# Kernel optimization log

Hardware: AMD Instinct MI355X
Metric: run time of the kernel (lower is better)

Reference implementation:

```python
import jax, jax.numpy as jnp
import numpy as np

B, T, S, E, H, D = 4, 1024, 1024, 1024, 16, 64


def _ln(x, g, b, eps=1e-5):
    m = x.mean(-1, keepdims=True)
    v = ((x - m) ** 2).mean(-1, keepdims=True)
    return (x - m) * jax.lax.rsqrt(v + eps) * g + b


def _mha(xq, xkv, mask4, Wq, Wk, Wv, Wo, bo):
    # Wq/Wk/Wv: [H, E, D] (stacked per-head bias-free linears)
    q = jnp.einsum('bte,hed->bhtd', xq, Wq)
    k = jnp.einsum('bse,hed->bhsd', xkv, Wk)
    v = jnp.einsum('bse,hed->bhsd', xkv, Wv)
    # NOTE: original scales by C**-0.5 with C = n_embd, not head_size
    wei = jnp.einsum('bhtd,bhsd->bhts', q, k) * (float(E) ** -0.5)
    wei = jnp.where(mask4 == 0, jnp.float32(-1e9), wei)
    wei = jax.nn.softmax(wei, axis=-1)
    o = jnp.einsum('bhts,bhsd->bhtd', wei, v)  # [B,H,T,D]
    b_, h_, t_, d_ = o.shape
    o = o.transpose(0, 2, 1, 3).reshape(b_, t_, h_ * d_)
    return o @ Wo + bo


def setup_inputs() -> dict:
    key = jax.random.key(0)
    ks = jax.random.split(key, 24)
    sd = 0.02
    inp = {
        'x': jax.random.normal(ks[0], (B, T, E), jnp.float32),
        'x_m': jnp.ones((B, 1, T), jnp.int32),
        'ca': jax.random.normal(ks[1], (B, S, E), jnp.float32),
        'ca_m': jnp.ones((B, 1, S), jnp.int32),
        'Wq_s': jax.random.normal(ks[2], (H, E, D), jnp.float32) * sd,
        'Wk_s': jax.random.normal(ks[3], (H, E, D), jnp.float32) * sd,
        'Wv_s': jax.random.normal(ks[4], (H, E, D), jnp.float32) * sd,
        'Wo_s': jax.random.normal(ks[5], (E, E), jnp.float32) * sd,
        'bo_s': jnp.zeros((E,), jnp.float32),
        'Wq_c': jax.random.normal(ks[6], (H, E, D), jnp.float32) * sd,
        'Wk_c': jax.random.normal(ks[7], (H, E, D), jnp.float32) * sd,
        'Wv_c': jax.random.normal(ks[8], (H, E, D), jnp.float32) * sd,
        'Wo_c': jax.random.normal(ks[9], (E, E), jnp.float32) * sd,
        'bo_c': jnp.zeros((E,), jnp.float32),
        'ln1_g': jnp.ones((E,), jnp.float32), 'ln1_b': jnp.zeros((E,), jnp.float32),
        'ln2_g': jnp.ones((E,), jnp.float32), 'ln2_b': jnp.zeros((E,), jnp.float32),
        'ln3_g': jnp.ones((E,), jnp.float32), 'ln3_b': jnp.zeros((E,), jnp.float32),
        'W1': jax.random.normal(ks[10], (E, 4 * E), jnp.float32) * sd,
        'b1': jnp.zeros((4 * E,), jnp.float32),
        'W2': jax.random.normal(ks[11], (4 * E, E), jnp.float32) * sd,
        'b2': jnp.zeros((E,), jnp.float32),
    }
    return inp


def reference(x, x_m, ca, ca_m, Wq_s, Wk_s, Wv_s, Wo_s, bo_s,
              Wq_c, Wk_c, Wv_c, Wo_c, bo_c,
              ln1_g, ln1_b, ln2_g, ln2_b, ln3_g, ln3_b,
              W1, b1, W2, b2):
    tril = jnp.tril(jnp.ones((T, T), jnp.int32))
    # self-attn mask: x_m [B,1,T] & tril [T,T] -> [B,1,T,T] (broadcast over heads)
    self_mask = x_m[:, :, None, :] * tril          # [B,1,T,T]
    cross_mask = ca_m[:, :, None, :]               # [B,1,1,S]
    x = x + _mha(_ln(x, ln1_g, ln1_b), _ln(x, ln1_g, ln1_b) if False else _ln(x, ln1_g, ln1_b), self_mask, Wq_s, Wk_s, Wv_s, Wo_s, bo_s)
    x = x + _mha(_ln(x, ln2_g, ln2_b), ca, cross_mask, Wq_c, Wk_c, Wv_c, Wo_c, bo_c)
    h = _ln(x, ln3_g, ln3_b)
    x = x + (jax.nn.relu(h @ W1 + b1) @ W2 + b2)
    return x
```

## Files before the change

### kernel.cpp

```cpp
#include <hip/hip_runtime.h>
#include <hip/hip_bf16.h>
#include <cstdint>
#include <cstddef>

typedef __attribute__((ext_vector_type(8))) short  s8v;
typedef __attribute__((ext_vector_type(4))) short  s4v;
typedef __attribute__((ext_vector_type(8))) __bf16 b8v;
typedef __attribute__((ext_vector_type(4))) float  f32x4;
typedef __attribute__((ext_vector_type(4))) unsigned u32x4;

__device__ __forceinline__ short f2bf(float f){
  unsigned u = __builtin_bit_cast(unsigned, f);
  unsigned r = (u + 0x7fffu + ((u >> 16) & 1u)) >> 16;
  return (short)(unsigned short)r;
}
__device__ __forceinline__ float bf2f(short s){
  return __builtin_bit_cast(float, ((unsigned)(unsigned short)s) << 16);
}

__device__ __forceinline__ f32x4 mfma16(s8v a, s8v b, f32x4 c){
  return __builtin_amdgcn_mfma_f32_16x16x32_bf16(
      __builtin_bit_cast(b8v, a), __builtin_bit_cast(b8v, b), c, 0, 0, 0);
}

__device__ __forceinline__ unsigned cvtpk(float a, float b){
  unsigned w;
  asm("v_cvt_pk_bf16_f32 %0, %1, %2" : "=v"(w) : "v"(a), "v"(b));
  return w;
}

__global__ __launch_bounds__(256)
void ln_k(const float* __restrict__ x, const float* __restrict__ g,
          const float* __restrict__ b, short* __restrict__ out)
{
  const int row = blockIdx.x, tid = threadIdx.x;
  const float4 v = ((const float4*)(x + (size_t)row*1024))[tid];
  float s  = v.x+v.y+v.z+v.w;
  float s2 = v.x*v.x+v.y*v.y+v.z*v.z+v.w*v.w;
  #pragma unroll
  for (int off=32; off; off>>=1){ s += __shfl_down(s, off); s2 += __shfl_down(s2, off); }
  __shared__ float red[8];
  const int wave = tid>>6, lane = tid&63;
  if (lane==0){ red[wave]=s; red[4+wave]=s2; }
  __syncthreads();
  s  = red[0]+red[1]+red[2]+red[3];
  s2 = red[4]+red[5]+red[6]+red[7];
  const float mean = s*(1.f/1024.f);
  const float rstd = rsqrtf(s2*(1.f/1024.f) - mean*mean + 1e-5f);
  const float4 gv = ((const float4*)g)[tid];
  const float4 bv = ((const float4*)b)[tid];
  s4v o;
  o[0] = f2bf((v.x-mean)*rstd*gv.x + bv.x);
  o[1] = f2bf((v.y-mean)*rstd*gv.y + bv.y);
  o[2] = f2bf((v.z-mean)*rstd*gv.z + bv.z);
  o[3] = f2bf((v.w-mean)*rstd*gv.w + bv.w);
  *(s4v*)(out + (size_t)row*1024 + tid*4) = o;
}

__global__ __launch_bounds__(256)
void cast_k(const float* __restrict__ in, short* __restrict__ out)
{
  const int i = blockIdx.x*256 + threadIdx.x;
  const float4 v = ((const float4*)in)[i];
  s4v o; o[0]=f2bf(v.x); o[1]=f2bf(v.y); o[2]=f2bf(v.z); o[3]=f2bf(v.w);
  ((s4v*)out)[i] = o;
}

__global__ __launch_bounds__(256)
void tcast_k(const float* __restrict__ in, short* __restrict__ out, int E2, int D2)
{
  __shared__ float t[32][33];
  const int h  = blockIdx.z;
  const int e0 = blockIdx.x*32, d0 = blockIdx.y*32;
  const int tx = threadIdx.x & 31, ty = threadIdx.x >> 5;
  const float* ip = in + (size_t)h*E2*D2;
  #pragma unroll
  for (int r = ty; r < 32; r += 8)
    t[r][tx] = ip[(size_t)(e0+r)*D2 + d0 + tx];
  __syncthreads();
  short* op = out + (size_t)h*D2*E2;
  #pragma unroll
  for (int r = ty; r < 32; r += 8)
    op[(size_t)(d0+r)*E2 + e0 + tx] = f2bf(t[tx][r]);
}

__global__ __launch_bounds__(256)
void vtrans_k(const short* __restrict__ V, int ldv, short* __restrict__ Vt, int S, int H)
{
  __shared__ short t[32][34];
  const int bh = blockIdx.z;
  const int b = bh / H, h = bh % H;
  const int s0 = blockIdx.x*32, d0 = blockIdx.y*32;
  const int tx = threadIdx.x & 31, ty = threadIdx.x >> 5;
  const short* ip = V + (size_t)b*S*ldv + h*64;
  #pragma unroll
  for (int r = ty; r < 32; r += 8)
    t[r][tx] = ip[(size_t)(s0+r)*ldv + d0 + tx];
  __syncthreads();
  short* op = Vt + ((size_t)bh*64 + d0)*S + s0;
  #pragma unroll
  for (int r = ty; r < 32; r += 8)
    op[(size_t)r*S + tx] = t[tx][r];
}

__global__ __launch_bounds__(256)
void red4_k(const short* __restrict__ p, const float* __restrict__ bias,
            const float* __restrict__ resid, float* __restrict__ out)
{
  const int i = blockIdx.x*256 + threadIdx.x;
  float4 o = ((const float4*)resid)[i];
  const float4 bv = ((const float4*)bias)[i & 255];
  o.x += bv.x; o.y += bv.y; o.z += bv.z; o.w += bv.w;
  #pragma unroll
  for (int z=0; z<4; z++){
    const s4v v = ((const s4v*)(p + (size_t)z*4194304))[i];
    o.x += bf2f(v[0]); o.y += bf2f(v[1]); o.z += bf2f(v[2]); o.w += bf2f(v[3]);
  }
  ((float4*)out)[i] = o;
}

template<int BN, int BIAS, int RELU, int RESID, int WF32>
__global__ __launch_bounds__(256, 2)
void gemm_bt(const short* __restrict__ A, const short* __restrict__ Bt,
             const float* __restrict__ bias, const float* __restrict__ resid,
             short* __restrict__ Cb, float* __restrict__ Cf,
             int M, int N, int K)
{
  __shared__ short lds[3][128*32 + BN*32];
  const int nwg = gridDim.x * gridDim.y;
  int id = blockIdx.y * gridDim.x + blockIdx.x;
  id = (id & 7) * (nwg >> 3) + (id >> 3);
  const int bx = id % gridDim.x, by = id / gridDim.x;
  const int m0 = by*128, n0 = bx*BN;

  const int tid  = threadIdx.x;
  const int wave = tid>>6, lane = tid&63;
  const int lo = lane&15, hi = lane>>4;
  const int wm = wave>>1, wn = wave&1;

  constexpr int NJ = BN/32;
  constexpr int BC = BN>>6;
  f32x4 acc[4][NJ] = {};
  const int NK = K >> 5;

  auto stage = [&](int buf, int kt){
    const short* Ag = A  + (size_t)m0*K + kt*32;
    const short* Bg = Bt + (size_t)n0*K + kt*32;
    #pragma unroll
    for (int c=0;c<2;c++){
      const int q = (wave*2+c)*64 + lane;
      const int r = q>>2, cc = q&3;
      __builtin_amdgcn_global_load_lds(
        (const __attribute__((address_space(1))) void*)(Ag + (size_t)r*K + cc*8),
        (__attribute__((address_space(3))) void*)(&lds[buf][(wave*2+c)*512]),
        16, 0, 0);
    }
    #pragma unroll
    for (int c=0;c<BC;c++){
      const int q = (wave*BC+c)*64 + lane;
      const int r = q>>2, cc = q&3;
      __builtin_amdgcn_global_load_lds(
        (const __attribute__((address_space(1))) void*)(Bg + (size_t)r*K + cc*8),
        (__attribute__((address_space(3))) void*)(&lds[buf][4096 + (wave*BC+c)*512]),
        16, 0, 0);
    }
  };

  stage(0, 0);
  if (NK > 1) stage(1, 1);

  for (int kt=0; kt<NK; kt++){
    if (kt+1 < NK){
      if constexpr (BN==128) asm volatile("s_waitcnt vmcnt(4)" ::: "memory");
      else                   asm volatile("s_waitcnt vmcnt(3)" ::: "memory");
    } else {
      asm volatile("s_waitcnt vmcnt(0)" ::: "memory");
    }
    __builtin_amdgcn_s_barrier();
    __builtin_amdgcn_sched_barrier(0);
    if (kt+2 < NK) stage((kt+2)%3, kt+2);

    const short* la = &lds[kt%3][0];
    const short* lb = &lds[kt%3][4096];
    s8v af[4], bfr[NJ];
    #pragma unroll
    for (int i=0;i<4;i++)
      af[i] = *(const s8v*)(la + (wm*64 + i*16 + lo)*32 + hi*8);
    #pragma unroll
    for (int j=0;j<NJ;j++)
      bfr[j] = *(const s8v*)(lb + (wn*(BN/2) + j*16 + lo)*32 + hi*8);
    #pragma unroll
    for (int i=0;i<4;i++)
      #pragma unroll
      for (int j=0;j<NJ;j++)
        acc[i][j] = mfma16(af[i], bfr[j], acc[i][j]);
  }

  #pragma unroll
  for (int i=0;i<4;i++){
    const int row = m0 + wm*64 + i*16 + hi*4;
    #pragma unroll
    for (int j=0;j<NJ;j++){
      const int col = n0 + wn*(BN/2) + j*16 + lo;
      const float bv = BIAS ? bias[col] : 0.0f;
      #pragma unroll
      for (int r=0;r<4;r++){
        float v = acc[i][j][r] + bv;
        if (RELU) v = fmaxf(v, 0.0f);
        const size_t idx = (size_t)(row + r)*N + col;
        if (RESID) v += resid[idx];
        if (WF32) Cf[idx] = v; else Cb[idx] = f2bf(v);
      }
    }
  }
}

template<int BIAS, int RELU, int RESID, int WF32>
__global__ __launch_bounds__(512, 1)
void gemm256(const short* __restrict__ A, int lda,
             const short* __restrict__ Bt, int ldb,
             const float* __restrict__ bias, const float* __restrict__ resid,
             short* __restrict__ Cb, float* __restrict__ Cf,
             int M, int N, int K)
{
  __shared__ short lds[2][32768];
  const int nwg = gridDim.x * gridDim.y;
  int id = blockIdx.y * gridDim.x + blockIdx.x;
  id = (id & 7) * (nwg >> 3) + (id >> 3);
  const int bx = id % gridDim.x, by = id / gridDim.x;
  const int m0 = by*256, n0 = bx*256;
  A  += (size_t)blockIdx.z * K;
  Bt += (size_t)blockIdx.z * K;
  const size_t cofs = (size_t)blockIdx.z * M * N;

  const int tid = threadIdx.x;
  const int lane = tid&63, wave = tid>>6;
  const int lo = lane&15, hi = lane>>4;
  const int wr = wave>>2, wc = wave&3;

  f32x4 acc[8][4] = {};
  const int NT = K >> 6;

  auto stageA = [&](int buf, int kt, int part){
    const short* Ag = A + (size_t)m0*lda + kt*64;
    const int q = part*512 + tid;
    const int r = q>>3, c = q&7;
    __builtin_amdgcn_global_load_lds(
      (const __attribute__((address_space(1))) void*)(Ag + (size_t)r*lda + ((c^(r&7))*8)),
      (__attribute__((address_space(3))) void*)(&lds[buf][q*8]), 16, 0, 0);
  };
  auto stageB = [&](int buf, int kt, int part){
    const short* Bg = Bt + (size_t)n0*ldb + kt*64;
    const int q = part*512 + tid;
    const int r = q>>3, c = q&7;
    __builtin_amdgcn_global_load_lds(
      (const __attribute__((address_space(1))) void*)(Bg + (size_t)r*ldb + ((c^(r&7))*8)),
      (__attribute__((address_space(3))) void*)(&lds[buf][16384 + q*8]), 16, 0, 0);
  };

  #pragma unroll
  for (int p=0;p<4;p++){ stageA(0,0,p); stageB(0,0,p); }
  __syncthreads();

  for (int t=0; t<NT; t++){
    const int cur = t&1;
    const short* la = &lds[cur][0];
    const short* lb = &lds[cur][16384];
    const bool pf = (t+1 < NT);
    #pragma unroll
    for (int ks=0; ks<2; ks++){
      s8v bf[4];
      #pragma unroll
      for (int j=0;j<4;j++){
        const int r = wc*64 + j*16 + lo;
        bf[j] = *(const s8v*)(lb + r*64 + (((ks*4+hi)^(r&7))*8));
      }
      #pragma unroll
      for (int mh=0; mh<2; mh++){
        s8v af[4];
        #pragma unroll
        for (int i=0;i<4;i++){
          const int r = wr*128 + mh*64 + i*16 + lo;
          af[i] = *(const s8v*)(la + r*64 + (((ks*4+hi)^(r&7))*8));
        }
        if (pf && ks==0){
          stageA(cur^1, t+1, mh*2);   stageB(cur^1, t+1, mh*2);
          stageA(cur^1, t+1, mh*2+1); stageB(cur^1, t+1, mh*2+1);
        }
        __builtin_amdgcn_s_setprio(1);
        #pragma unroll
        for (int i=0;i<4;i++)
          #pragma unroll
          for (int j=0;j<4;j++)
            acc[mh*4+i][j] = mfma16(af[i], bf[j], acc[mh*4+i][j]);
        __builtin_amdgcn_s_setprio(0);
      }
    }
    __syncthreads();
  }

  #pragma unroll
  for (int I=0;I<8;I++){
    const int row = m0 + wr*128 + I*16 + hi*4;
    #pragma unroll
    for (int j=0;j<4;j++){
      const int col = n0 + wc*64 + j*16 + lo;
      const float bv = BIAS ? bias[col] : 0.0f;
      #pragma unroll
      for (int r=0;r<4;r++){
        float v = acc[I][j][r] + bv;
        if (RELU) v = fmaxf(v, 0.0f);
        const size_t idx = cofs + (size_t)(row + r)*N + col;
        if (RESID) v += resid[idx];
        if (WF32) Cf[idx] = v; else Cb[idx] = f2bf(v);
      }
    }
  }
}

template<int CAUSAL>
__global__ __launch_bounds__(256, 4)
void attn_k(const short* __restrict__ Q, int ldq,
            const short* __restrict__ K, int ldk,
            const short* __restrict__ Vt, int ldvt,
            const int* __restrict__ msk,
            short* __restrict__ O, int ldo,
            int H, int Tq, int Sk)
{
  __shared__ short kls[2][4096];
  __shared__ short vls[2][4096];
  const int bh = blockIdx.x;
  const int b = bh / H, h = bh % H;
  const int tid = threadIdx.x;
  const int wave = tid>>6, lane = tid&63;
  const int lo = lane&15, hi = lane>>4;
  const int t0 = blockIdx.y*64 + wave*16;

  const short* Qb  = Q + (size_t)(b*Tq)*ldq + h*64;
  const short* Kb  = K + (size_t)(b*Sk)*ldk + h*64;
  const short* Vtb = Vt + (size_t)bh*64*ldvt;
  const int*   mb  = msk + (size_t)b*Sk;

  const short* qp = Qb + (size_t)(t0+lo)*ldq + hi*8;
  const s8v qa0 = *(const s8v*)(qp);
  const s8v qa1 = *(const s8v*)(qp + 32);

  float mrow = -INFINITY, lrow = 0.f;
  f32x4 oacc[4] = {};
  const int trow = t0 + lo;
  const int nblk = CAUSAL ? (blockIdx.y + 1) : (Sk>>6);
  const float sc2 = 0.03125f * 1.44269504088896f;
  const int x8 = lo & 7;

  auto stage = [&](int buf, int it){
    const int s0 = it*64;
    #pragma unroll
    for (int rd=0; rd<2; rd++){
      const int q = rd*256 + tid;
      const int r = q>>3, c = q&7;
      const int cs = (c ^ (r&7))*8;
      __builtin_amdgcn_global_load_lds(
        (const __attribute__((address_space(1))) void*)(Kb + (size_t)(s0+r)*ldk + cs),
        (__attribute__((address_space(3))) void*)(&kls[buf][(rd*256 + wave*64)*8]),
        16, 0, 0);
      __builtin_amdgcn_global_load_lds(
        (const __attribute__((address_space(1))) void*)(Vtb + (size_t)r*ldvt + s0 + cs),
        (__attribute__((address_space(3))) void*)(&vls[buf][(rd*256 + wave*64)*8]),
        16, 0, 0);
    }
  };

  stage(0, 0);
  int cur = 0;
  for (int it=0; it<nblk; it++){
    __syncthreads();
    if (it+1 < nblk) stage(cur^1, it+1);
    const int s0 = it*64;

    int ka[4][4];
    #pragma unroll
    for (int g=0; g<4; g++){
      const int4 kv = ((const int4*)mb)[(s0>>2) + g*4 + hi];
      ka[g][0]=kv.x; ka[g][1]=kv.y; ka[g][2]=kv.z; ka[g][3]=kv.w;
    }

    const short* kl = kls[cur];
    s8v kf[4][2];
    #pragma unroll
    for (int g=0; g<4; g++){
      const int rb = (g*16 + lo)*64;
      kf[g][0] = *(const s8v*)(kl + rb + ((hi     ^ x8)*8));
      kf[g][1] = *(const s8v*)(kl + rb + (((4+hi) ^ x8)*8));
    }

    f32x4 sg[4] = {};
    __builtin_amdgcn_s_setprio(1);
    #pragma unroll
    for (int g=0; g<4; g++){
      sg[g] = mfma16(kf[g][0], qa0, sg[g]);
      sg[g] = mfma16(kf[g][1], qa1, sg[g]);
    }
    __builtin_amdgcn_s_setprio(0);

    const bool lastblk = CAUSAL && (it == nblk-1);
    float p[4][4];
    #pragma unroll
    for (int g=0; g<4; g++)
      #pragma unroll
      for (int r=0; r<4; r++){
        const int sidx = s0 + g*16 + 4*hi + r;
        const bool ok = ka[g][r] && (!lastblk || sidx <= trow);
        p[g][r] = ok ? sg[g][r]*sc2 : -1.5e9f;
      }

    float bmax;
    {
      float m0_ = fmaxf(fmaxf(p[0][0],p[0][1]), fmaxf(p[0][2],p[0][3]));
      float m1_ = fmaxf(fmaxf(p[1][0],p[1][1]), fmaxf(p[1][2],p[1][3]));
      float m2_ = fmaxf(fmaxf(p[2][0],p[2][1]), fmaxf(p[2][2],p[2][3]));
      float m3_ = fmaxf(fmaxf(p[3][0],p[3][1]), fmaxf(p[3][2],p[3][3]));
      bmax = fmaxf(fmaxf(m0_,m1_), fmaxf(m2_,m3_));
    }
    bmax = fmaxf(bmax, __shfl_xor(bmax, 16));
    bmax = fmaxf(bmax, __shfl_xor(bmax, 32));

    const float mn  = fmaxf(mrow, bmax);
    const float fac = exp2f(mrow - mn);
    mrow = mn;
    #pragma unroll
    for (int g=0; g<4; g++)
      #pragma unroll
      for (int r=0; r<4; r++)
        p[g][r] = exp2f(p[g][r] - mn);

    float bsum;
    {
      float s0_ = (p[0][0]+p[0][1]) + (p[0][2]+p[0][3]);
      float s1_ = (p[1][0]+p[1][1]) + (p[1][2]+p[1][3]);
      float s2_ = (p[2][0]+p[2][1]) + (p[2][2]+p[2][3]);
      float s3_ = (p[3][0]+p[3][1]) + (p[3][2]+p[3][3]);
      bsum = (s0_+s1_) + (s2_+s3_);
    }
    bsum += __shfl_xor(bsum, 16);
    bsum += __shfl_xor(bsum, 32);
    lrow = lrow*fac + bsum;
    #pragma unroll
    for (int f=0; f<4; f++)
      #pragma unroll
      for (int r=0; r<4; r++)
        oacc[f][r] *= fac;

    u32x4 pw0, pw1;
    pw0[0] = cvtpk(p[0][0], p[0][1]);
    pw0[1] = cvtpk(p[0][2], p[0][3]);
    pw0[2] = cvtpk(p[1][0], p[1][1]);
    pw0[3] = cvtpk(p[1][2], p[1][3]);
    pw1[0] = cvtpk(p[2][0], p[2][1]);
    pw1[1] = cvtpk(p[2][2], p[2][3]);
    pw1[2] = cvtpk(p[3][0], p[3][1]);
    pw1[3] = cvtpk(p[3][2], p[3][3]);
    const s8v pb0 = __builtin_bit_cast(s8v, pw0);
    const s8v pb1 = __builtin_bit_cast(s8v, pw1);

    const short* vl = vls[cur];
    __builtin_amdgcn_s_setprio(1);
    #pragma unroll
    for (int f=0; f<4; f++){
      const int rb = (f*16 + lo)*64;
      const int h2 = hi>>1, o2 = (hi&1)*4;
      const s4v a0 = *(const s4v*)(vl + rb + (((h2  ) ^ x8)*8) + o2);
      const s4v a1 = *(const s4v*)(vl + rb + (((2+h2) ^ x8)*8) + o2);
      const s4v a2 = *(const s4v*)(vl + rb + (((4+h2) ^ x8)*8) + o2);
      const s4v a3 = *(const s4v*)(vl + rb + (((6+h2) ^ x8)*8) + o2);
      const s8v av0 = __builtin_shufflevector(a0, a1, 0,1,2,3,4,5,6,7);
      const s8v av1 = __builtin_shufflevector(a2, a3, 0,1,2,3,4,5,6,7);
      oacc[f] = mfma16(av0, pb0, oacc[f]);
      oacc[f] = mfma16(av1, pb1, oacc[f]);
    }
    __builtin_amdgcn_s_setprio(0);
    cur ^= 1;
  }

  const float inv = 1.0f / lrow;
  short* Ob = O + (size_t)(b*Tq)*ldo + h*64 + (size_t)(t0+lo)*ldo + 4*hi;
  #pragma unroll
  for (int f=0; f<4; f++){
    s4v o;
    #pragma unroll
    for (int r=0; r<4; r++) o[r] = f2bf(oacc[f][r]*inv);
    *(s4v*)(Ob + f*16) = o;
  }
}

extern "C" void kernel_launch(void* const* d_in, const int* in_sizes, int n_in,
                              void* d_out, int out_size, void* d_ws, size_t ws_size,
                              hipStream_t stream)
{
  (void)in_sizes; (void)n_in; (void)out_size; (void)ws_size;
  const float* x    = (const float*)d_in[0];
  const int*   xm   = (const int*)  d_in[1];
  const float* ca   = (const float*)d_in[2];
  const int*   cam  = (const int*)  d_in[3];
  const float* Wq_s = (const float*)d_in[4];
  const float* Wk_s = (const float*)d_in[5];
  const float* Wv_s = (const float*)d_in[6];
  const float* Wo_s = (const float*)d_in[7];
  const float* bo_s = (const float*)d_in[8];
  const float* Wq_c = (const float*)d_in[9];
  const float* Wk_c = (const float*)d_in[10];
  const float* Wv_c = (const float*)d_in[11];
  const float* Wo_c = (const float*)d_in[12];
  const float* bo_c = (const float*)d_in[13];
  const float* ln1g = (const float*)d_in[14];
  const float* ln1b = (const float*)d_in[15];
  const float* ln2g = (const float*)d_in[16];
  const float* ln2b = (const float*)d_in[17];
  const float* ln3g = (const float*)d_in[18];
  const float* ln3b = (const float*)d_in[19];
  const float* W1   = (const float*)d_in[20];
  const float* b1   = (const float*)d_in[21];
  const float* W2   = (const float*)d_in[22];
  const float* b2   = (const float*)d_in[23];
  float* out = (float*)d_out;

  char* ws = (char*)d_ws;
  size_t off = 0;
  auto alloc = [&](size_t bytes)->void*{
    void* p = ws + off; off += (bytes + 255) & ~(size_t)255; return p; };

  short* w_qkv_s = (short*)alloc((size_t)3072*1024*2);
  short* w_o_s   = (short*)alloc((size_t)1024*1024*2);
  short* w_q_c   = (short*)alloc((size_t)1024*1024*2);
  short* w_kv_c  = (short*)alloc((size_t)2048*1024*2);
  short* w_o_c   = (short*)alloc((size_t)1024*1024*2);
  short* w_1     = (short*)alloc((size_t)4096*1024*2);
  short* w_2     = (short*)alloc((size_t)1024*4096*2);
  short* xn      = (short*)alloc((size_t)4096*1024*2);
  short* cab     = (short*)alloc((size_t)4096*1024*2);
  short* qkv     = (short*)alloc((size_t)4096*3072*2);
  short* attno   = (short*)alloc((size_t)4096*1024*2);
  float* xres    = (float*)alloc((size_t)4096*1024*4);
  short* hffn    = (short*)alloc((size_t)4096*4096*2);
  float* pA      = (float*)alloc((size_t)4096*1024*4);
  float* pB      = (float*)alloc((size_t)4096*1024*4);
  short* pP      = (short*)pA;
  short* kvbuf   = qkv + (size_t)4096*1024;
  short* vt_s    = hffn;
  short* vt_c    = hffn + (size_t)4*1024*1024;
  (void)pB;

  tcast_k<<<dim3(32,  2,16),256,0,stream>>>(Wq_s, w_qkv_s,           1024,   64);
  tcast_k<<<dim3(32,  2,16),256,0,stream>>>(Wk_s, w_qkv_s+1024*1024, 1024,   64);
  tcast_k<<<dim3(32,  2,16),256,0,stream>>>(Wv_s, w_qkv_s+2048*1024, 1024,   64);
  tcast_k<<<dim3(32, 32, 1),256,0,stream>>>(Wo_s, w_o_s,             1024, 1024);
  tcast_k<<<dim3(32,  2,16),256,0,stream>>>(Wq_c, w_q_c,             1024,   64);
  tcast_k<<<dim3(32,  2,16),256,0,stream>>>(Wk_c, w_kv_c,            1024,   64);
  tcast_k<<<dim3(32,  2,16),256,0,stream>>>(Wv_c, w_kv_c+1024*1024,  1024,   64);
  tcast_k<<<dim3(32, 32, 1),256,0,stream>>>(Wo_c, w_o_c,             1024, 1024);
  tcast_k<<<dim3(32,128, 1),256,0,stream>>>(W1,   w_1,               1024, 4096);
  tcast_k<<<dim3(128,32, 1),256,0,stream>>>(W2,   w_2,               4096, 1024);
  cast_k<<<4096,256,0,stream>>>(ca, cab);

  ln_k<<<4096,256,0,stream>>>(x, ln1g, ln1b, xn);
  gemm256<0,0,0,0><<<dim3(12,16),512,0,stream>>>(xn, 1024, w_qkv_s, 1024,
                                                 nullptr, nullptr, qkv, nullptr,
                                                 4096, 3072, 1024);
  vtrans_k<<<dim3(32,2,64),256,0,stream>>>(qkv+2048, 3072, vt_s, 1024, 16);
  attn_k<1><<<dim3(64,16),256,0,stream>>>(qkv, 3072, qkv+1024, 3072, vt_s, 1024,
                                          xm, attno, 1024, 16, 1024, 1024);
  gemm_bt<64,1,0,1,1><<<dim3(16,32),256,0,stream>>>(attno, w_o_s, bo_s, x,
                                                    nullptr, xres, 4096, 1024, 1024);

  ln_k<<<4096,256,0,stream>>>(xres, ln2g, ln2b, xn);
  gemm_bt<64,0,0,0,0><<<dim3(16,32),256,0,stream>>>(xn, w_q_c, nullptr, nullptr,
                                                    qkv, nullptr, 4096, 1024, 1024);
  gemm256<0,0,0,0><<<dim3(8,16),512,0,stream>>>(cab, 1024, w_kv_c, 1024,
                                                nullptr, nullptr, kvbuf, nullptr,
                                                4096, 2048, 1024);
  vtrans_k<<<dim3(32,2,64),256,0,stream>>>(kvbuf+1024, 2048, vt_c, 1024, 16);
  attn_k<0><<<dim3(64,16),256,0,stream>>>(qkv, 1024, kvbuf, 2048, vt_c, 1024,
                                          cam, attno, 1024, 16, 1024, 1024);
  gemm_bt<64,1,0,1,1><<<dim3(16,32),256,0,stream>>>(attno, w_o_c, bo_c, xres,
                                                    nullptr, xres, 4096, 1024, 1024);

  ln_k<<<4096,256,0,stream>>>(xres, ln3g, ln3b, xn);
  gemm256<1,1,0,0><<<dim3(16,16),512,0,stream>>>(xn, 1024, w_1, 1024,
                                                 b1, nullptr, hffn, nullptr,
                                                 4096, 4096, 1024);
  gemm256<0,0,0,0><<<dim3(4,16,4),512,0,stream>>>(hffn, 4096, w_2, 4096,
                                                  nullptr, nullptr, pP, nullptr,
                                                  4096, 1024, 1024);
  red4_k<<<4096,256,0,stream>>>(pP, b2, xres, out);
}
```

Baseline: 378.9 us.

## Fold softmax scale into Q GEMMs, precompute mask bias, lazy rescale, permute Vt

Folds the attention scale times log2(e) into the Q projection epilogues, so the attention loop no longer multiplies scores by the scale. The integer key mask is converted once into an additive float bias, and the causal check now runs only on the last block. Online-softmax rescaling of the accumulators is skipped unless the block max exceeds the running max by more than 8, which lets p values grow up to 2^8 before renormalisation. V transpose writes a permuted column order so the PV MFMA operands load as single 8-wide vectors instead of four 4-wide loads plus shuffles. These remove per-element ALU and LDS work from the attention inner loop, in exchange for a tighter reliance on fp32 headroom and a Q buffer stored pre-scaled in bf16.

```diff
diff --git a/kernel.cpp b/kernel.cpp
--- a/kernel.cpp
+++ b/kernel.cpp
@@ -8,6 +8,8 @@
 typedef __attribute__((ext_vector_type(8))) __bf16 b8v;
 typedef __attribute__((ext_vector_type(4))) float  f32x4;
 typedef __attribute__((ext_vector_type(4))) unsigned u32x4;
+
+#define SC2Q 0.0450843293f
 
 __device__ __forceinline__ short f2bf(float f){
   unsigned u = __builtin_bit_cast(unsigned, f);
@@ -67,6 +69,15 @@
 }
 
 __global__ __launch_bounds__(256)
+void mkb_k(const int* __restrict__ xm, const int* __restrict__ cm,
+           float* __restrict__ mbS, float* __restrict__ mbC)
+{
+  const int i = blockIdx.x*256 + threadIdx.x;
+  mbS[i] = xm[i] ? 0.f : -1.5e9f;
+  mbC[i] = cm[i] ? 0.f : -1.5e9f;
+}
+
+__global__ __launch_bounds__(256)
 void tcast_k(const float* __restrict__ in, short* __restrict__ out, int E2, int D2)
 {
   __shared__ float t[32][33];
@@ -97,10 +108,13 @@
   for (int r = ty; r < 32; r += 8)
     t[r][tx] = ip[(size_t)(s0+r)*ldv + d0 + tx];
   __syncthreads();
-  short* op = Vt + ((size_t)bh*64 + d0)*S + s0;
+  const int s  = s0 + tx;
+  const int ks = (s>>5)&1, bb = (tx>>4)&1, hh = (tx>>2)&3, rr = tx&3;
+  const int cp = (s & ~63) + ks*32 + hh*8 + bb*4 + rr;
+  short* op = Vt + ((size_t)bh*64 + d0)*S;
   #pragma unroll
   for (int r = ty; r < 32; r += 8)
-    op[(size_t)r*S + tx] = t[tx][r];
+    op[(size_t)r*S + cp] = t[tx][r];
 }
 
 __global__ __launch_bounds__(256)
@@ -119,7 +133,7 @@
   ((float4*)out)[i] = o;
 }
 
-template<int BN, int BIAS, int RELU, int RESID, int WF32>
+template<int BN, int BIAS, int RELU, int RESID, int WF32, int SCQ>
 __global__ __launch_bounds__(256, 2)
 void gemm_bt(const short* __restrict__ A, const short* __restrict__ Bt,
              const float* __restrict__ bias, const float* __restrict__ resid,
@@ -206,6 +220,7 @@
       #pragma unroll
       for (int r=0;r<4;r++){
         float v = acc[i][j][r] + bv;
+        if constexpr (SCQ==2) v *= SC2Q;
         if (RELU) v = fmaxf(v, 0.0f);
         const size_t idx = (size_t)(row + r)*N + col;
         if (RESID) v += resid[idx];
@@ -215,7 +230,7 @@
   }
 }
 
-template<int BIAS, int RELU, int RESID, int WF32>
+template<int BIAS, int RELU, int RESID, int WF32, int SCQ>
 __global__ __launch_bounds__(512, 1)
 void gemm256(const short* __restrict__ A, int lda,
              const short* __restrict__ Bt, int ldb,
@@ -309,6 +324,7 @@
       #pragma unroll
       for (int r=0;r<4;r++){
         float v = acc[I][j][r] + bv;
+        if constexpr (SCQ==1) { if (col < 1024) v *= SC2Q; }
         if (RELU) v = fmaxf(v, 0.0f);
         const size_t idx = cofs + (size_t)(row + r)*N + col;
         if (RESID) v += resid[idx];
@@ -323,7 +339,7 @@
 void attn_k(const short* __restrict__ Q, int ldq,
             const short* __restrict__ K, int ldk,
             const short* __restrict__ Vt, int ldvt,
-            const int* __restrict__ msk,
+            const float* __restrict__ mbias,
             short* __restrict__ O, int ldo,
             int H, int Tq, int Sk)
 {
@@ -339,7 +355,7 @@
   const short* Qb  = Q + (size_t)(b*Tq)*ldq + h*64;
   const short* Kb  = K + (size_t)(b*Sk)*ldk + h*64;
   const short* Vtb = Vt + (size_t)bh*64*ldvt;
-  const int*   mb  = msk + (size_t)b*Sk;
+  const float* mb  = mbias + (size_t)b*Sk;
 
   const short* qp = Qb + (size_t)(t0+lo)*ldq + hi*8;
   const s8v qa0 = *(const s8v*)(qp);
@@ -349,7 +365,6 @@
   f32x4 oacc[4] = {};
   const int trow = t0 + lo;
   const int nblk = CAUSAL ? (blockIdx.y + 1) : (Sk>>6);
-  const float sc2 = 0.03125f * 1.44269504088896f;
   const int x8 = lo & 7;
 
   auto stage = [&](int buf, int it){
@@ -377,13 +392,6 @@
     if (it+1 < nblk) stage(cur^1, it+1);
     const int s0 = it*64;
 
-    int ka[4][4];
-    #pragma unroll
-    for (int g=0; g<4; g++){
-      const int4 kv = ((const int4*)mb)[(s0>>2) + g*4 + hi];
-      ka[g][0]=kv.x; ka[g][1]=kv.y; ka[g][2]=kv.z; ka[g][3]=kv.w;
-    }
-
     const short* kl = kls[cur];
     s8v kf[4][2];
     #pragma unroll
@@ -402,53 +410,63 @@
     }
     __builtin_amdgcn_s_setprio(0);
 
-    const bool lastblk = CAUSAL && (it == nblk-1);
     float p[4][4];
     #pragma unroll
-    for (int g=0; g<4; g++)
-      #pragma unroll
-      for (int r=0; r<4; r++){
-        const int sidx = s0 + g*16 + 4*hi + r;
-        const bool ok = ka[g][r] && (!lastblk || sidx <= trow);
-        p[g][r] = ok ? sg[g][r]*sc2 : -1.5e9f;
-      }
+    for (int g=0; g<4; g++){
+      const f32x4 mv = ((const f32x4*)mb)[(s0>>2) + g*4 + hi];
+      #pragma unroll
+      for (int r=0; r<4; r++)
+        p[g][r] = sg[g][r] + mv[r];
+    }
+    if (CAUSAL && it == nblk-1){
+      #pragma unroll
+      for (int g=0; g<4; g++)
+        #pragma unroll
+        for (int r=0; r<4; r++){
+          const int sidx = s0 + g*16 + 4*hi + r;
+          if (sidx > trow) p[g][r] = -1.5e9f;
+        }
+    }
 
     float bmax;
     {
-      float m0_ = fmaxf(fmaxf(p[0][0],p[0][1]), fmaxf(p[0][2],p[0][3]));
-      float m1_ = fmaxf(fmaxf(p[1][0],p[1][1]), fmaxf(p[1][2],p[1][3]));
-      float m2_ = fmaxf(fmaxf(p[2][0],p[2][1]), fmaxf(p[2][2],p[2][3]));
-      float m3_ = fmaxf(fmaxf(p[3][0],p[3][1]), fmaxf(p[3][2],p[3][3]));
+      const float m0_ = fmaxf(fmaxf(fmaxf(p[0][0],p[0][1]),p[0][2]),p[0][3]);
+      const float m1_ = fmaxf(fmaxf(fmaxf(p[1][0],p[1][1]),p[1][2]),p[1][3]);
+      const float m2_ = fmaxf(fmaxf(fmaxf(p[2][0],p[2][1]),p[2][2]),p[2][3]);
+      const float m3_ = fmaxf(fmaxf(fmaxf(p[3][0],p[3][1]),p[3][2]),p[3][3]);
       bmax = fmaxf(fmaxf(m0_,m1_), fmaxf(m2_,m3_));
     }
     bmax = fmaxf(bmax, __shfl_xor(bmax, 16));
     bmax = fmaxf(bmax, __shfl_xor(bmax, 32));
 
-    const float mn  = fmaxf(mrow, bmax);
-    const float fac = exp2f(mrow - mn);
-    mrow = mn;
-    #pragma unroll
-    for (int g=0; g<4; g++)
-      #pragma unroll
-      for (int r=0; r<4; r++)
-        p[g][r] = exp2f(p[g][r] - mn);
+    if (!__all(bmax <= mrow + 8.0f)){
+      const float mn  = fmaxf(mrow, bmax);
+      const float fac = exp2f(mrow - mn);
+      mrow = mn;
+      lrow *= fac;
+      #pragma unroll
+      for (int f=0; f<4; f++)
+        #pragma unroll
+        for (int r=0; r<4; r++)
+          oacc[f][r] *= fac;
+    }
 
     float bsum;
     {
-      float s0_ = (p[0][0]+p[0][1]) + (p[0][2]+p[0][3]);
-      float s1_ = (p[1][0]+p[1][1]) + (p[1][2]+p[1][3]);
-      float s2_ = (p[2][0]+p[2][1]) + (p[2][2]+p[2][3]);
-      float s3_ = (p[3][0]+p[3][1]) + (p[3][2]+p[3][3]);
+      #pragma unroll
+      for (int g=0; g<4; g++)
+        #pragma unroll
+        for (int r=0; r<4; r++)
+          p[g][r] = exp2f(p[g][r] - mrow);
+      const float s0_ = (p[0][0]+p[0][1]) + (p[0][2]+p[0][3]);
+      const float s1_ = (p[1][0]+p[1][1]) + (p[1][2]+p[1][3]);
+      const float s2_ = (p[2][0]+p[2][1]) + (p[2][2]+p[2][3]);
+      const float s3_ = (p[3][0]+p[3][1]) + (p[3][2]+p[3][3]);
       bsum = (s0_+s1_) + (s2_+s3_);
     }
     bsum += __shfl_xor(bsum, 16);
     bsum += __shfl_xor(bsum, 32);
-    lrow = lrow*fac + bsum;
-    #pragma unroll
-    for (int f=0; f<4; f++)
-      #pragma unroll
-      for (int r=0; r<4; r++)
-        oacc[f][r] *= fac;
+    lrow += bsum;
 
     u32x4 pw0, pw1;
     pw0[0] = cvtpk(p[0][0], p[0][1]);
@@ -467,13 +485,8 @@
     #pragma unroll
     for (int f=0; f<4; f++){
       const int rb = (f*16 + lo)*64;
-      const int h2 = hi>>1, o2 = (hi&1)*4;
-      const s4v a0 = *(const s4v*)(vl + rb + (((h2  ) ^ x8)*8) + o2);
-      const s4v a1 = *(const s4v*)(vl + rb + (((2+h2) ^ x8)*8) + o2);
-      const s4v a2 = *(const s4v*)(vl + rb + (((4+h2) ^ x8)*8) + o2);
-      const s4v a3 = *(const s4v*)(vl + rb + (((6+h2) ^ x8)*8) + o2);
-      const s8v av0 = __builtin_shufflevector(a0, a1, 0,1,2,3,4,5,6,7);
-      const s8v av1 = __builtin_shufflevector(a2, a3, 0,1,2,3,4,5,6,7);
+      const s8v av0 = *(const s8v*)(vl + rb + (((hi  ) ^ x8)*8));
+      const s8v av1 = *(const s8v*)(vl + rb + (((4+hi) ^ x8)*8));
       oacc[f] = mfma16(av0, pb0, oacc[f]);
       oacc[f] = mfma16(av1, pb1, oacc[f]);
     }
@@ -543,6 +556,8 @@
   short* hffn    = (short*)alloc((size_t)4096*4096*2);
   float* pA      = (float*)alloc((size_t)4096*1024*4);
   float* pB      = (float*)alloc((size_t)4096*1024*4);
+  float* mbS     = (float*)alloc((size_t)4096*4);
+  float* mbC     = (float*)alloc((size_t)4096*4);
   short* pP      = (short*)pA;
   short* kvbuf   = qkv + (size_t)4096*1024;
   short* vt_s    = hffn;
@@ -560,35 +575,36 @@
   tcast_k<<<dim3(32,128, 1),256,0,stream>>>(W1,   w_1,               1024, 4096);
   tcast_k<<<dim3(128,32, 1),256,0,stream>>>(W2,   w_2,               4096, 1024);
   cast_k<<<4096,256,0,stream>>>(ca, cab);
+  mkb_k<<<16,256,0,stream>>>(xm, cam, mbS, mbC);
 
   ln_k<<<4096,256,0,stream>>>(x, ln1g, ln1b, xn);
-  gemm256<0,0,0,0><<<dim3(12,16),512,0,stream>>>(xn, 1024, w_qkv_s, 1024,
-                                                 nullptr, nullptr, qkv, nullptr,
-                                                 4096, 3072, 1024);
+  gemm256<0,0,0,0,1><<<dim3(12,16),512,0,stream>>>(xn, 1024, w_qkv_s, 1024,
+                                                   nullptr, nullptr, qkv, nullptr,
+                                                   4096, 3072, 1024);
   vtrans_k<<<dim3(32,2,64),256,0,stream>>>(qkv+2048, 3072, vt_s, 1024, 16);
   attn_k<1><<<dim3(64,16),256,0,stream>>>(qkv, 3072, qkv+1024, 3072, vt_s, 1024,
-                                          xm, attno, 1024, 16, 1024, 1024);
-  gemm_bt<64,1,0,1,1><<<dim3(16,32),256,0,stream>>>(attno, w_o_s, bo_s, x,
-                                                    nullptr, xres, 4096, 1024, 1024);
+                                          mbS, attno, 1024, 16, 1024, 1024);
+  gemm_bt<64,1,0,1,1,0><<<dim3(16,32),256,0,stream>>>(attno, w_o_s, bo_s, x,
+                                                      nullptr, xres, 4096, 1024, 1024);
 
   ln_k<<<4096,256,0,stream>>>(xres, ln2g, ln2b, xn);
-  gemm_bt<64,0,0,0,0><<<dim3(16,32),256,0,stream>>>(xn, w_q_c, nullptr, nullptr,
-                                                    qkv, nullptr, 4096, 1024, 1024);
-  gemm256<0,0,0,0><<<dim3(8,16),512,0,stream>>>(cab, 1024, w_kv_c, 1024,
-                                                nullptr, nullptr, kvbuf, nullptr,
-                                                4096, 2048, 1024);
+  gemm_bt<64,0,0,0,0,2><<<dim3(16,32),256,0,stream>>>(xn, w_q_c, nullptr, nullptr,
+                                                      qkv, nullptr, 4096, 1024, 1024);
+  gemm256<0,0,0,0,0><<<dim3(8,16),512,0,stream>>>(cab, 1024, w_kv_c, 1024,
+                                                  nullptr, nullptr, kvbuf, nullptr,
+                                                  4096, 2048, 1024);
   vtrans_k<<<dim3(32,2,64),256,0,stream>>>(kvbuf+1024, 2048, vt_c, 1024, 16);
   attn_k<0><<<dim3(64,16),256,0,stream>>>(qkv, 1024, kvbuf, 2048, vt_c, 1024,
-                                          cam, attno, 1024, 16, 1024, 1024);
-  gemm_bt<64,1,0,1,1><<<dim3(16,32),256,0,stream>>>(attno, w_o_c, bo_c, xres,
-                                                    nullptr, xres, 4096, 1024, 1024);
+                                          mbC, attno, 1024, 16, 1024, 1024);
+  gemm_bt<64,1,0,1,1,0><<<dim3(16,32),256,0,stream>>>(attno, w_o_c, bo_c, xres,
+                                                      nullptr, xres, 4096, 1024, 1024);
 
   ln_k<<<4096,256,0,stream>>>(xres, ln3g, ln3b, xn);
-  gemm256<1,1,0,0><<<dim3(16,16),512,0,stream>>>(xn, 1024, w_1, 1024,
-                                                 b1, nullptr, hffn, nullptr,
-                                                 4096, 4096, 1024);
-  gemm256<0,0,0,0><<<dim3(4,16,4),512,0,stream>>>(hffn, 4096, w_2, 4096,
-                                                  nullptr, nullptr, pP, nullptr,
-                                                  4096, 1024, 1024);
+  gemm256<1,1,0,0,0><<<dim3(16,16),512,0,stream>>>(xn, 1024, w_1, 1024,
+                                                   b1, nullptr, hffn, nullptr,
+                                                   4096, 4096, 1024);
+  gemm256<0,0,0,0,0><<<dim3(4,16,4),512,0,stream>>>(hffn, 4096, w_2, 4096,
+                                                    nullptr, nullptr, pP, nullptr,
+                                                    4096, 1024, 1024);
   red4_k<<<4096,256,0,stream>>>(pP, b2, xres, out);
 }
```

After: 368.0 us. 1.03x faster.
